# Optimization experiments

Measured on AMD Instinct MI355X. Metric: run time of the kernel, lower is better.

## Reference

```python
import jax, jax.numpy as jnp
import numpy as np

B, S, D, H = 2, 2048, 1024, 16
HD = D // H  # 64
LN_EPS = 1e-5


def setup_inputs() -> dict:
    key = jax.random.key(0)
    ks = jax.random.split(key, 10)
    s = 0.02
    return {
        "x": jax.random.normal(ks[0], (B, S, D), jnp.float32),
        "cdr_bias": jax.random.normal(ks[1], (B, S), jnp.float32),
        "Wq": jax.random.normal(ks[2], (D, D), jnp.float32) * s,
        "bq": jnp.zeros((D,), jnp.float32),
        "Wk": jax.random.normal(ks[3], (D, D), jnp.float32) * s,
        "bk": jnp.zeros((D,), jnp.float32),
        "Wv": jax.random.normal(ks[4], (D, D), jnp.float32) * s,
        "bv": jnp.zeros((D,), jnp.float32),
        "Wo": jax.random.normal(ks[5], (D, D), jnp.float32) * s,
        "bo": jnp.zeros((D,), jnp.float32),
        "gamma": jnp.ones((D,), jnp.float32),
        "beta": jnp.zeros((D,), jnp.float32),
        "cdr_weight": jnp.asarray(1.0, jnp.float32),
    }


def _rotate_half(t):
    # interleaved rotate: [-x2_0, x1_0, -x2_1, x1_1, ...] matching torch stack+reshape
    t1 = t[..., ::2]
    t2 = t[..., 1::2]
    return jnp.stack((-t2, t1), axis=-1).reshape(t.shape)


def reference(x, cdr_bias, Wq, bq, Wk, bk, Wv, bv, Wo, bo, gamma, beta, cdr_weight):
    b, s, d = x.shape

    # RoPE tables (faithful to original: sin/cos concatenated, rotate_half interleaved)
    pos = jnp.arange(s, dtype=x.dtype)
    inv_freq = 1.0 / (10000.0 ** (jnp.arange(0, HD, 2, dtype=x.dtype) / HD))
    sinusoid = pos[:, None] * inv_freq[None, :]              # [S, HD/2]
    sin_pos = jnp.concatenate([jnp.sin(sinusoid)] * 2, -1)   # [S, HD]
    cos_pos = jnp.concatenate([jnp.cos(sinusoid)] * 2, -1)
    sin_pos = sin_pos[None, None]                            # [1,1,S,HD]
    cos_pos = cos_pos[None, None]

    def heads(t):
        return t.reshape(b, s, H, HD).transpose(0, 2, 1, 3)  # [B,H,S,HD]

    Q = heads(x @ Wq + bq)
    K = heads(x @ Wk + bk)
    V = heads(x @ Wv + bv)

    Q = Q * cos_pos + _rotate_half(Q) * sin_pos
    K = K * cos_pos + _rotate_half(K) * sin_pos

    scores = jnp.einsum("bhqd,bhkd->bhqk", Q, K) / jnp.sqrt(jnp.asarray(HD, x.dtype))
    scores = scores + cdr_bias[:, None, None, :] * cdr_weight  # additive key-side bias
    probs = jax.nn.softmax(scores, axis=-1)                    # dropout = identity (eval)

    attn = jnp.einsum("bhqk,bhkd->bhqd", probs, V)
    attn = attn.transpose(0, 2, 1, 3).reshape(b, s, d)
    out = attn @ Wo + bo

    res = x + out
    mu = jnp.mean(res, axis=-1, keepdims=True)
    var = jnp.mean(jnp.square(res - mu), axis=-1, keepdims=True)
    return (res - mu) / jnp.sqrt(var + LN_EPS) * gamma + beta
```

## Files before the change

### kernel.cpp

```cpp
#include <hip/hip_runtime.h>
#include <hip/hip_bf16.h>
#include <math.h>

#define BB 2
#define SS 2048
#define DD 1024
#define HH 16
#define HD 64
#define MM (BB*SS)
#define LN_EPS 1e-5f
#define KVB 64
#define LOG2E 1.44269504088896340736f

typedef unsigned short u16;
typedef __attribute__((ext_vector_type(8))) short short8;
typedef __attribute__((ext_vector_type(4))) float f32x4;
typedef __attribute__((ext_vector_type(4))) unsigned short u16x4;

__device__ __forceinline__ u16 f2bf(float f) {
    union { __hip_bfloat16 h; u16 u; } cv;
    cv.h = __float2bfloat16(f);
    return cv.u;
}

__device__ __forceinline__ float exp2_(float x) {
    float r;
    asm("v_exp_f32 %0, %1" : "=v"(r) : "v"(x));
    return r;
}

__device__ __forceinline__ void gload16(const void* g, void* l) {
    __builtin_amdgcn_global_load_lds(
        (const __attribute__((address_space(1))) void*)g,
        (__attribute__((address_space(3))) void*)l, 16, 0, 0);
}

__global__ __launch_bounds__(256) void k_prep(
        const float* __restrict__ x,
        const float* __restrict__ Wq, const float* __restrict__ Wk,
        const float* __restrict__ Wv, const float* __restrict__ Wo,
        const float* __restrict__ cdr_bias, const float* __restrict__ cw,
        u16* __restrict__ xb, u16* __restrict__ wqkvt, u16* __restrict__ wot,
        float* __restrict__ cosb, float* __restrict__ sinb, float* __restrict__ biasf) {
    __shared__ float t[32][33];
    int bz = blockIdx.x, tid = threadIdx.x;
    if (bz < 4096) {
        int i = bz * 256 + tid;
        float4 v = ((const float4*)x)[i];
        u16x4 o;
        o[0] = f2bf(v.x); o[1] = f2bf(v.y); o[2] = f2bf(v.z); o[3] = f2bf(v.w);
        ((u16x4*)xb)[i] = o;
    } else if (bz < 8192) {
        int zb = bz - 4096;
        int z = zb >> 10, rem = zb & 1023;
        int k0 = (rem & 31) * 32, n0 = (rem >> 5) * 32;
        const float* W = (z == 0) ? Wq : (z == 1) ? Wk : (z == 2) ? Wv : Wo;
        u16* dst = (z < 3) ? (wqkvt + (size_t)z * DD * DD) : wot;
        int tx = tid & 31, ty = tid >> 5;
        #pragma unroll
        for (int r = 0; r < 32; r += 8)
            t[ty + r][tx] = W[(size_t)(k0 + ty + r) * DD + n0 + tx];
        __syncthreads();
        #pragma unroll
        for (int r = 0; r < 32; r += 8)
            dst[(size_t)(n0 + ty + r) * DD + k0 + tx] = f2bf(t[tx][ty + r]);
    } else {
        int idx = (bz - 8192) * 256 + tid;
        if (idx < BB * SS) biasf[idx] = cdr_bias[idx] * cw[0] * LOG2E;
        int s = idx >> 6, j = idx & 63;
        double invf = pow(10000.0, -((double)(2 * (j & 31))) / 64.0);
        double ang = (double)s * invf;
        cosb[idx] = (float)cos(ang);
        sinb[idx] = (float)sin(ang);
    }
}

#define STAGE_T(A_PTR, B_PTR, T)                                               \
    {                                                                          \
        u16* Ab = Alds + ((T) % 3) * 4096;                                     \
        u16* Bb = Blds + ((T) % 3) * 4096;                                     \
        _Pragma("unroll")                                                      \
        for (int i_ = 0; i_ < 2; i_++) {                                       \
            int p_ = i_ * 256 + tid;                                           \
            int row_ = p_ >> 2, c_ = p_ & 3;                                   \
            gload16(A_PTR + (size_t)(bm + row_) * DD + (T) * 32 + ((c_ ^ (row_ & 3)) << 3), Ab + p_ * 8); \
            gload16(B_PTR + (size_t)(bn + row_) * DD + (T) * 32 + ((c_ ^ (row_ & 3)) << 3), Bb + p_ * 8); \
        }                                                                      \
    }

#define GEMM_PIPE3(A_PTR, B_PTR)                                               \
    f32x4 acc[4][4] = {};                                                      \
    STAGE_T(A_PTR, B_PTR, 0)                                                   \
    STAGE_T(A_PTR, B_PTR, 1)                                                   \
    for (int kt = 0; kt < 32; kt++) {                                          \
        if (kt < 31) asm volatile("s_waitcnt vmcnt(4)" ::: "memory");          \
        else         asm volatile("s_waitcnt vmcnt(0)" ::: "memory");          \
        __builtin_amdgcn_s_barrier();                                          \
        const u16* Acur = Alds + (kt % 3) * 4096;                              \
        const u16* Bcur = Blds + (kt % 3) * 4096;                              \
        short8 a[4], b[4];                                                     \
        int rch = (lg ^ (lr & 3)) << 3;                                        \
        _Pragma("unroll")                                                      \
        for (int i = 0; i < 4; i++) {                                          \
            a[i] = *(const short8*)(Acur + (wm * 64 + i * 16 + lr) * 32 + rch); \
            b[i] = *(const short8*)(Bcur + (wn * 64 + i * 16 + lr) * 32 + rch); \
        }                                                                      \
        if (kt + 2 < 32) STAGE_T(A_PTR, B_PTR, kt + 2)                         \
        __builtin_amdgcn_s_setprio(1);                                         \
        _Pragma("unroll")                                                      \
        for (int i = 0; i < 4; i++)                                            \
            _Pragma("unroll")                                                  \
            for (int j = 0; j < 4; j++)                                        \
                acc[i][j] = __builtin_amdgcn_mfma_f32_16x16x32_bf16(a[i], b[j], acc[i][j], 0, 0, 0); \
        __builtin_amdgcn_s_setprio(0);                                         \
    }                                                                          \
    __syncthreads();

__global__ __launch_bounds__(256, 3) void k_gemm_qkv(
        const u16* __restrict__ xb, const u16* __restrict__ wqkvt,
        const float* __restrict__ bq, const float* __restrict__ bk, const float* __restrict__ bv,
        const float* __restrict__ cosb, const float* __restrict__ sinb,
        u16* __restrict__ q, u16* __restrict__ k, u16* __restrict__ vt) {
    __shared__ u16 SMEM[24576];
    u16* Alds = SMEM;
    u16* Blds = SMEM + 12288;
    int tid = threadIdx.x;
    int lane = tid & 63, wid = tid >> 6;
    int wm = wid >> 1, wn = wid & 1;
    int bm = blockIdx.x * 128, bn = blockIdx.y * 128;
    int lr = lane & 15, lg = lane >> 4;

    GEMM_PIPE3(xb, wqkvt)

    int w = bn >> 10;
    if (w == 2) {
        u16* Tr = SMEM;
        #pragma unroll
        for (int j = 0; j < 4; j++) {
            int n_l = wn * 64 + j * 16 + lr;
            float bias = bv[(bn - 2048) + n_l];
            #pragma unroll
            for (int i = 0; i < 4; i++) {
                ushort4 pk;
                pk.x = f2bf(acc[i][j][0] + bias);
                pk.y = f2bf(acc[i][j][1] + bias);
                pk.z = f2bf(acc[i][j][2] + bias);
                pk.w = f2bf(acc[i][j][3] + bias);
                *(ushort4*)&Tr[n_l * 136 + wm * 64 + i * 16 + lg * 4] = pk;
            }
        }
        __syncthreads();
        int n_r = tid >> 1, hf = tid & 1;
        int nglob = (bn - 2048) + n_r;
        int b_ = bm >> 11;
        size_t vbase = ((size_t)(b_ * HH + (nglob >> 6)) * HD + (nglob & 63)) * SS
                     + (bm & 2047) + hf * 64;
        #pragma unroll
        for (int ii = 0; ii < 8; ii++)
            *(short8*)(vt + vbase + ii * 8) = *(const short8*)&Tr[n_r * 136 + hf * 64 + ii * 8];
    } else {
        int m0 = bm + wm * 64, n0 = bn + wn * 64;
        #pragma unroll
        for (int j = 0; j < 4; j++) {
            int n = n0 + j * 16 + lr;
            int n1 = n & 1023;
            int h = n1 >> 6, d = n1 & 63;
            float bias = (w == 0) ? bq[n1] : bk[n1];
            #pragma unroll
            for (int i = 0; i < 4; i++) {
                #pragma unroll
                for (int r = 0; r < 4; r++) {
                    int m = m0 + i * 16 + lg * 4 + r;
                    int b_ = m >> 11, s = m & 2047;
                    float val = acc[i][j][r] + bias;
                    float part = __shfl_xor(val, 1);
                    float c = cosb[s * 64 + d], sn = sinb[s * 64 + d];
                    float rot = (d & 1) ? part : -part;
                    val = val * c + rot * sn;
                    size_t bh = (size_t)(b_ * HH + h);
                    if (w == 0)
                        q[(bh * SS + s) * HD + d] = f2bf(val * (0.125f * LOG2E));
                    else
                        k[(bh * SS + s) * HD + d] = f2bf(val);
                }
            }
        }
    }
}

__global__ __launch_bounds__(256, 3) void k_gemm_o(
        const u16* __restrict__ attnb, const u16* __restrict__ wot,
        const float* __restrict__ bo, const float* __restrict__ x,
        float* __restrict__ res) {
    __shared__ u16 SMEM[24576];
    u16* Alds = SMEM;
    u16* Blds = SMEM + 12288;
    int tid = threadIdx.x;
    int lane = tid & 63, wid = tid >> 6;
    int wm = wid >> 1, wn = wid & 1;
    int bm = blockIdx.x * 128, bn = blockIdx.y * 128;
    int lr = lane & 15, lg = lane >> 4;

    GEMM_PIPE3(attnb, wot)

    int m0 = bm + wm * 64, n0 = bn + wn * 64;
    #pragma unroll
    for (int i = 0; i < 4; i++) {
        #pragma unroll
        for (int j = 0; j < 4; j++) {
            int n = n0 + j * 16 + lr;
            #pragma unroll
            for (int r = 0; r < 4; r++) {
                int m = m0 + i * 16 + lg * 4 + r;
                res[(size_t)m * DD + n] = acc[i][j][r] + bo[n] + x[(size_t)m * DD + n];
            }
        }
    }
}

__device__ __forceinline__ void stage64x64(const u16* __restrict__ gbase, size_t rstride,
                                           u16* lds, int tid) {
    int row = tid >> 3, c = tid & 7;
    gload16(gbase + (size_t)row * rstride + (size_t)((c ^ (row & 7)) << 3), lds + tid * 8);
}

__global__ __launch_bounds__(512, 4) void k_attn(
        const u16* __restrict__ q, const u16* __restrict__ kkv, const u16* __restrict__ vt,
        const float* __restrict__ biasf, u16* __restrict__ attnb) {
    __shared__ u16 Klds[2][64 * 64];
    __shared__ u16 Vlds[2][64 * 64];
    __shared__ u16 plds[8][16][72];

    int tid = threadIdx.x;
    int lane = tid & 63, wid = tid >> 6;
    int flat = blockIdx.y * gridDim.x + blockIdx.x;
    int bh = (flat & 7) * 4 + (flat >> 7);
    int qb = (flat >> 3) & 15;
    int b_ = bh >> 4, h = bh & 15;
    int q0 = qb * 128 + wid * 16;
    int lr = lane & 15, lg = lane >> 4;

    short8 qa[2];
    #pragma unroll
    for (int ks = 0; ks < 2; ks++)
        qa[ks] = *(const short8*)(q + ((size_t)bh * SS + q0 + lr) * HD + ks * 32 + lg * 8);

    stage64x64(kkv + ((size_t)bh * SS) * HD, HD, Klds[0], tid);
    stage64x64(vt + ((size_t)bh * HD) * SS, SS, Vlds[0], tid);
    __syncthreads();

    f32x4 acco[4] = {};
    f32x4 acS = {};
    const float* bias_b = biasf + (size_t)b_ * SS;
    short8 vone;
    #pragma unroll
    for (int j = 0; j < 8; j++) vone[j] = (short)0x3F80;

    for (int t = 0; t < SS / KVB; t++) {
        int cur = t & 1;
        if (t + 1 < SS / KVB) {
            int kv1 = (t + 1) * KVB;
            stage64x64(kkv + ((size_t)bh * SS + kv1) * HD, HD, Klds[cur ^ 1], tid);
            stage64x64(vt + ((size_t)bh * HD) * SS + kv1, SS, Vlds[cur ^ 1], tid);
        }
        const u16* Kc = Klds[cur];
        const u16* Vc = Vlds[cur];

        f32x4 s_[4];
        #pragma unroll
        for (int n = 0; n < 4; n++) {
            float4 b4 = *(const float4*)(bias_b + t * KVB + n * 16 + lg * 4);
            s_[n][0] = b4.x; s_[n][1] = b4.y; s_[n][2] = b4.z; s_[n][3] = b4.w;
        }

        short8 kf[4][2], vf[4][2];
        #pragma unroll
        for (int n = 0; n < 4; n++) {
            int row = n * 16 + lr;
            #pragma unroll
            for (int ks = 0; ks < 2; ks++)
                kf[n][ks] = *(const short8*)(Kc + row * 64 + (((ks * 4 + lg) ^ (lr & 7)) << 3));
        }
        #pragma unroll
        for (int dt = 0; dt < 4; dt++) {
            int row = dt * 16 + lr;
            #pragma unroll
            for (int kt = 0; kt < 2; kt++)
                vf[dt][kt] = *(const short8*)(Vc + row * 64 + (((kt * 4 + lg) ^ (lr & 7)) << 3));
        }

        __builtin_amdgcn_s_setprio(1);
        #pragma unroll
        for (int n = 0; n < 4; n++) {
            s_[n] = __builtin_amdgcn_mfma_f32_16x16x32_bf16(kf[n][0], qa[0], s_[n], 0, 0, 0);
            s_[n] = __builtin_amdgcn_mfma_f32_16x16x32_bf16(kf[n][1], qa[1], s_[n], 0, 0, 0);
        }
        __builtin_amdgcn_s_setprio(0);

        #pragma unroll
        for (int n = 0; n < 4; n++) {
            ushort4 pk;
            pk.x = f2bf(exp2_(s_[n][0]));
            pk.y = f2bf(exp2_(s_[n][1]));
            pk.z = f2bf(exp2_(s_[n][2]));
            pk.w = f2bf(exp2_(s_[n][3]));
            *(ushort4*)&plds[wid][lr][n * 16 + lg * 4] = pk;
        }
        asm volatile("s_waitcnt lgkmcnt(0)" ::: "memory");
        __builtin_amdgcn_s_setprio(1);
        #pragma unroll
        for (int kt = 0; kt < 2; kt++) {
            short8 pa = *(const short8*)&plds[wid][lr][kt * 32 + lg * 8];
            #pragma unroll
            for (int dt = 0; dt < 4; dt++)
                acco[dt] = __builtin_amdgcn_mfma_f32_16x16x32_bf16(pa, vf[dt][kt], acco[dt], 0, 0, 0);
            acS = __builtin_amdgcn_mfma_f32_16x16x32_bf16(pa, vone, acS, 0, 0, 0);
        }
        __builtin_amdgcn_s_setprio(0);
        __syncthreads();
    }

    float linv[4];
    #pragma unroll
    for (int r = 0; r < 4; r++) linv[r] = 1.f / acS[r];
    #pragma unroll
    for (int dt = 0; dt < 4; dt++)
        #pragma unroll
        for (int r = 0; r < 4; r++)
            attnb[((size_t)b_ * SS + q0 + lg * 4 + r) * DD + h * HD + dt * 16 + lr] =
                f2bf(acco[dt][r] * linv[r]);
}

__global__ __launch_bounds__(256) void k_ln(const float* __restrict__ res,
        const float* __restrict__ gamma, const float* __restrict__ beta,
        float* __restrict__ out) {
    int row = blockIdx.x, tid = threadIdx.x;
    float4 v = ((const float4*)(res + (size_t)row * DD))[tid];
    float s = v.x + v.y + v.z + v.w;
    float ss = v.x * v.x + v.y * v.y + v.z * v.z + v.w * v.w;
    #pragma unroll
    for (int off = 32; off; off >>= 1) { s += __shfl_xor(s, off); ss += __shfl_xor(ss, off); }
    __shared__ float sbuf[8];
    int wid = tid >> 6, lane = tid & 63;
    if (lane == 0) { sbuf[wid] = s; sbuf[4 + wid] = ss; }
    __syncthreads();
    s = sbuf[0] + sbuf[1] + sbuf[2] + sbuf[3];
    ss = sbuf[4] + sbuf[5] + sbuf[6] + sbuf[7];
    float mu = s * (1.f / DD);
    float var = ss * (1.f / DD) - mu * mu;
    float rstd = rsqrtf(var + LN_EPS);
    float4 g = ((const float4*)gamma)[tid];
    float4 be = ((const float4*)beta)[tid];
    float4 o;
    o.x = (v.x - mu) * rstd * g.x + be.x;
    o.y = (v.y - mu) * rstd * g.y + be.y;
    o.z = (v.z - mu) * rstd * g.z + be.z;
    o.w = (v.w - mu) * rstd * g.w + be.w;
    ((float4*)(out + (size_t)row * DD))[tid] = o;
}

extern "C" void kernel_launch(void* const* d_in, const int* in_sizes, int n_in,
                              void* d_out, int out_size, void* d_ws, size_t ws_size,
                              hipStream_t stream) {
    const float* x        = (const float*)d_in[0];
    const float* cdr_bias = (const float*)d_in[1];
    const float* Wq       = (const float*)d_in[2];
    const float* bq       = (const float*)d_in[3];
    const float* Wk       = (const float*)d_in[4];
    const float* bk       = (const float*)d_in[5];
    const float* Wv       = (const float*)d_in[6];
    const float* bv       = (const float*)d_in[7];
    const float* Wo       = (const float*)d_in[8];
    const float* bo       = (const float*)d_in[9];
    const float* gamma    = (const float*)d_in[10];
    const float* beta     = (const float*)d_in[11];
    const float* cw       = (const float*)d_in[12];

    char* ws = (char*)d_ws;
    const size_t MB = 1048576;
    u16*   xb     = (u16*)(ws + 0);
    u16*   wqkvt  = (u16*)(ws + 8 * MB);
    u16*   wot    = (u16*)(ws + 14 * MB);
    u16*   qb     = (u16*)(ws + 16 * MB);
    u16*   kb     = (u16*)(ws + 24 * MB);
    u16*   vtb    = (u16*)(ws + 32 * MB);
    u16*   attnb  = (u16*)(ws + 40 * MB);
    float* res    = (float*)(ws + 48 * MB);
    float* biasf  = (float*)(ws + 48 * MB);
    float* cosb   = (float*)(ws + 64 * MB);
    float* sinb   = (float*)(ws + 64 * MB + 524288);

    k_prep     <<<8704, 256, 0, stream>>>(x, Wq, Wk, Wv, Wo, cdr_bias, cw,
                                          xb, wqkvt, wot, cosb, sinb, biasf);
    k_gemm_qkv <<<dim3(32, 24), 256, 0, stream>>>(xb, wqkvt, bq, bk, bv, cosb, sinb, qb, kb, vtb);
    k_attn     <<<dim3(16, 32), 512, 0, stream>>>(qb, kb, vtb, biasf, attnb);
    k_gemm_o   <<<dim3(32, 8), 256, 0, stream>>>(attnb, wot, bo, x, res);
    k_ln       <<<4096, 256, 0, stream>>>(res, gamma, beta, (float*)d_out);
}
```

Before: 123.7 us.

## Process two 16-row query fragments per wave in attention with 256-thread blocks

The attention kernel now runs 4 waves per block instead of 8, and each wave handles 32 query rows as two 16-row fragments. The K/V fragments read from LDS are reused across both fragments, which halves LDS fragment reads and the per-block staging thread count. The cost is more registers per wave (two sets of accumulators and Q fragments), a launch bound of 2 blocks per CU, and less wave-level parallelism for hiding latency.

```diff
diff --git a/kernel.cpp b/kernel.cpp
--- a/kernel.cpp
+++ b/kernel.cpp
@@ -218,18 +218,22 @@
     }
 }
 
-__device__ __forceinline__ void stage64x64(const u16* __restrict__ gbase, size_t rstride,
-                                           u16* lds, int tid) {
-    int row = tid >> 3, c = tid & 7;
-    gload16(gbase + (size_t)row * rstride + (size_t)((c ^ (row & 7)) << 3), lds + tid * 8);
-}
-
-__global__ __launch_bounds__(512, 4) void k_attn(
+__device__ __forceinline__ void stage64x64_256(const u16* __restrict__ gbase, size_t rstride,
+                                               u16* lds, int tid) {
+    #pragma unroll
+    for (int i = 0; i < 2; i++) {
+        int L = i * 256 + tid;
+        int row = L >> 3, c = L & 7;
+        gload16(gbase + (size_t)row * rstride + (size_t)((c ^ (row & 7)) << 3), lds + L * 8);
+    }
+}
+
+__global__ __launch_bounds__(256, 2) void k_attn(
         const u16* __restrict__ q, const u16* __restrict__ kkv, const u16* __restrict__ vt,
         const float* __restrict__ biasf, u16* __restrict__ attnb) {
     __shared__ u16 Klds[2][64 * 64];
     __shared__ u16 Vlds[2][64 * 64];
-    __shared__ u16 plds[8][16][72];
+    __shared__ u16 plds[4][32][72];
 
     int tid = threadIdx.x;
     int lane = tid & 63, wid = tid >> 6;
@@ -237,20 +241,22 @@
     int bh = (flat & 7) * 4 + (flat >> 7);
     int qb = (flat >> 3) & 15;
     int b_ = bh >> 4, h = bh & 15;
-    int q0 = qb * 128 + wid * 16;
+    int q0 = qb * 128 + wid * 32;
     int lr = lane & 15, lg = lane >> 4;
 
-    short8 qa[2];
-    #pragma unroll
-    for (int ks = 0; ks < 2; ks++)
-        qa[ks] = *(const short8*)(q + ((size_t)bh * SS + q0 + lr) * HD + ks * 32 + lg * 8);
-
-    stage64x64(kkv + ((size_t)bh * SS) * HD, HD, Klds[0], tid);
-    stage64x64(vt + ((size_t)bh * HD) * SS, SS, Vlds[0], tid);
+    short8 qa[2][2];
+    #pragma unroll
+    for (int qf = 0; qf < 2; qf++)
+        #pragma unroll
+        for (int ks = 0; ks < 2; ks++)
+            qa[qf][ks] = *(const short8*)(q + ((size_t)bh * SS + q0 + qf * 16 + lr) * HD + ks * 32 + lg * 8);
+
+    stage64x64_256(kkv + ((size_t)bh * SS) * HD, HD, Klds[0], tid);
+    stage64x64_256(vt + ((size_t)bh * HD) * SS, SS, Vlds[0], tid);
     __syncthreads();
 
-    f32x4 acco[4] = {};
-    f32x4 acS = {};
+    f32x4 acco[2][4] = {};
+    f32x4 acS[2] = {};
     const float* bias_b = biasf + (size_t)b_ * SS;
     short8 vone;
     #pragma unroll
@@ -260,18 +266,16 @@
         int cur = t & 1;
         if (t + 1 < SS / KVB) {
             int kv1 = (t + 1) * KVB;
-            stage64x64(kkv + ((size_t)bh * SS + kv1) * HD, HD, Klds[cur ^ 1], tid);
-            stage64x64(vt + ((size_t)bh * HD) * SS + kv1, SS, Vlds[cur ^ 1], tid);
+            stage64x64_256(kkv + ((size_t)bh * SS + kv1) * HD, HD, Klds[cur ^ 1], tid);
+            stage64x64_256(vt + ((size_t)bh * HD) * SS + kv1, SS, Vlds[cur ^ 1], tid);
         }
         const u16* Kc = Klds[cur];
         const u16* Vc = Vlds[cur];
 
-        f32x4 s_[4];
-        #pragma unroll
-        for (int n = 0; n < 4; n++) {
-            float4 b4 = *(const float4*)(bias_b + t * KVB + n * 16 + lg * 4);
-            s_[n][0] = b4.x; s_[n][1] = b4.y; s_[n][2] = b4.z; s_[n][3] = b4.w;
-        }
+        float4 bb[4];
+        #pragma unroll
+        for (int n = 0; n < 4; n++)
+            bb[n] = *(const float4*)(bias_b + t * KVB + n * 16 + lg * 4);
 
         short8 kf[4][2], vf[4][2];
         #pragma unroll
@@ -289,46 +293,57 @@
                 vf[dt][kt] = *(const short8*)(Vc + row * 64 + (((kt * 4 + lg) ^ (lr & 7)) << 3));
         }
 
-        __builtin_amdgcn_s_setprio(1);
-        #pragma unroll
-        for (int n = 0; n < 4; n++) {
-            s_[n] = __builtin_amdgcn_mfma_f32_16x16x32_bf16(kf[n][0], qa[0], s_[n], 0, 0, 0);
-            s_[n] = __builtin_amdgcn_mfma_f32_16x16x32_bf16(kf[n][1], qa[1], s_[n], 0, 0, 0);
-        }
-        __builtin_amdgcn_s_setprio(0);
-
-        #pragma unroll
-        for (int n = 0; n < 4; n++) {
-            ushort4 pk;
-            pk.x = f2bf(exp2_(s_[n][0]));
-            pk.y = f2bf(exp2_(s_[n][1]));
-            pk.z = f2bf(exp2_(s_[n][2]));
-            pk.w = f2bf(exp2_(s_[n][3]));
-            *(ushort4*)&plds[wid][lr][n * 16 + lg * 4] = pk;
-        }
-        asm volatile("s_waitcnt lgkmcnt(0)" ::: "memory");
-        __builtin_amdgcn_s_setprio(1);
-        #pragma unroll
-        for (int kt = 0; kt < 2; kt++) {
-            short8 pa = *(const short8*)&plds[wid][lr][kt * 32 + lg * 8];
-            #pragma unroll
-            for (int dt = 0; dt < 4; dt++)
-                acco[dt] = __builtin_amdgcn_mfma_f32_16x16x32_bf16(pa, vf[dt][kt], acco[dt], 0, 0, 0);
-            acS = __builtin_amdgcn_mfma_f32_16x16x32_bf16(pa, vone, acS, 0, 0, 0);
-        }
-        __builtin_amdgcn_s_setprio(0);
+        #pragma unroll
+        for (int qf = 0; qf < 2; qf++) {
+            f32x4 s_[4];
+            #pragma unroll
+            for (int n = 0; n < 4; n++) {
+                s_[n][0] = bb[n].x; s_[n][1] = bb[n].y; s_[n][2] = bb[n].z; s_[n][3] = bb[n].w;
+            }
+            __builtin_amdgcn_s_setprio(1);
+            #pragma unroll
+            for (int n = 0; n < 4; n++) {
+                s_[n] = __builtin_amdgcn_mfma_f32_16x16x32_bf16(kf[n][0], qa[qf][0], s_[n], 0, 0, 0);
+                s_[n] = __builtin_amdgcn_mfma_f32_16x16x32_bf16(kf[n][1], qa[qf][1], s_[n], 0, 0, 0);
+            }
+            __builtin_amdgcn_s_setprio(0);
+
+            #pragma unroll
+            for (int n = 0; n < 4; n++) {
+                ushort4 pk;
+                pk.x = f2bf(exp2_(s_[n][0]));
+                pk.y = f2bf(exp2_(s_[n][1]));
+                pk.z = f2bf(exp2_(s_[n][2]));
+                pk.w = f2bf(exp2_(s_[n][3]));
+                *(ushort4*)&plds[wid][qf * 16 + lr][n * 16 + lg * 4] = pk;
+            }
+            asm volatile("s_waitcnt lgkmcnt(0)" ::: "memory");
+            __builtin_amdgcn_s_setprio(1);
+            #pragma unroll
+            for (int kt = 0; kt < 2; kt++) {
+                short8 pa = *(const short8*)&plds[wid][qf * 16 + lr][kt * 32 + lg * 8];
+                #pragma unroll
+                for (int dt = 0; dt < 4; dt++)
+                    acco[qf][dt] = __builtin_amdgcn_mfma_f32_16x16x32_bf16(pa, vf[dt][kt], acco[qf][dt], 0, 0, 0);
+                acS[qf] = __builtin_amdgcn_mfma_f32_16x16x32_bf16(pa, vone, acS[qf], 0, 0, 0);
+            }
+            __builtin_amdgcn_s_setprio(0);
+        }
         __syncthreads();
     }
 
-    float linv[4];
-    #pragma unroll
-    for (int r = 0; r < 4; r++) linv[r] = 1.f / acS[r];
-    #pragma unroll
-    for (int dt = 0; dt < 4; dt++)
-        #pragma unroll
-        for (int r = 0; r < 4; r++)
-            attnb[((size_t)b_ * SS + q0 + lg * 4 + r) * DD + h * HD + dt * 16 + lr] =
-                f2bf(acco[dt][r] * linv[r]);
+    #pragma unroll
+    for (int qf = 0; qf < 2; qf++) {
+        float linv[4];
+        #pragma unroll
+        for (int r = 0; r < 4; r++) linv[r] = 1.f / acS[qf][r];
+        #pragma unroll
+        for (int dt = 0; dt < 4; dt++)
+            #pragma unroll
+            for (int r = 0; r < 4; r++)
+                attnb[((size_t)b_ * SS + q0 + qf * 16 + lg * 4 + r) * DD + h * HD + dt * 16 + lr] =
+                    f2bf(acco[qf][dt][r] * linv[r]);
+    }
 }
 
 __global__ __launch_bounds__(256) void k_ln(const float* __restrict__ res,
@@ -393,7 +408,7 @@
     k_prep     <<<8704, 256, 0, stream>>>(x, Wq, Wk, Wv, Wo, cdr_bias, cw,
                                           xb, wqkvt, wot, cosb, sinb, biasf);
     k_gemm_qkv <<<dim3(32, 24), 256, 0, stream>>>(xb, wqkvt, bq, bk, bv, cosb, sinb, qb, kb, vtb);
-    k_attn     <<<dim3(16, 32), 512, 0, stream>>>(qb, kb, vtb, biasf, attnb);
+    k_attn     <<<dim3(16, 32), 256, 0, stream>>>(qb, kb, vtb, biasf, attnb);
     k_gemm_o   <<<dim3(32, 8), 256, 0, stream>>>(attnb, wot, bo, x, res);
     k_ln       <<<4096, 256, 0, stream>>>(res, gamma, beta, (float*)d_out);
 }
```

Result: no change. 125.4 us (+1.4%).

## Load K/V fragments directly from global memory in attention, drop LDS staging

Applied to the files above, without the earlier changes.

The attention kernel no longer stages K and V tiles through double-buffered shared memory. Each wave now loads its MFMA fragments straight from global memory, relying on L1/L2 to serve the reuse across the block's waves. Blocks shrink to 256 threads covering 64 query rows, the grid doubles, and the per-tile __syncthreads is removed. This cuts LDS traffic and barrier stalls, but each wave now issues more global loads with no explicit prefetch, so latency hiding depends on occupancy.

```diff
diff --git a/kernel.cpp b/kernel.cpp
--- a/kernel.cpp
+++ b/kernel.cpp
@@ -218,75 +218,57 @@
     }
 }
 
-__device__ __forceinline__ void stage64x64(const u16* __restrict__ gbase, size_t rstride,
-                                           u16* lds, int tid) {
-    int row = tid >> 3, c = tid & 7;
-    gload16(gbase + (size_t)row * rstride + (size_t)((c ^ (row & 7)) << 3), lds + tid * 8);
-}
-
-__global__ __launch_bounds__(512, 4) void k_attn(
+__global__ __launch_bounds__(256, 4) void k_attn(
         const u16* __restrict__ q, const u16* __restrict__ kkv, const u16* __restrict__ vt,
         const float* __restrict__ biasf, u16* __restrict__ attnb) {
-    __shared__ u16 Klds[2][64 * 64];
-    __shared__ u16 Vlds[2][64 * 64];
-    __shared__ u16 plds[8][16][72];
+    __shared__ u16 plds[4][16][72];
 
     int tid = threadIdx.x;
     int lane = tid & 63, wid = tid >> 6;
     int flat = blockIdx.y * gridDim.x + blockIdx.x;
-    int bh = (flat & 7) * 4 + (flat >> 7);
-    int qb = (flat >> 3) & 15;
+    int w_ = flat >> 3;
+    int bh = (flat & 7) * 4 + (w_ >> 5);
+    int qb = w_ & 31;
     int b_ = bh >> 4, h = bh & 15;
-    int q0 = qb * 128 + wid * 16;
+    int q0 = qb * 64 + wid * 16;
     int lr = lane & 15, lg = lane >> 4;
 
     short8 qa[2];
     #pragma unroll
     for (int ks = 0; ks < 2; ks++)
         qa[ks] = *(const short8*)(q + ((size_t)bh * SS + q0 + lr) * HD + ks * 32 + lg * 8);
-
-    stage64x64(kkv + ((size_t)bh * SS) * HD, HD, Klds[0], tid);
-    stage64x64(vt + ((size_t)bh * HD) * SS, SS, Vlds[0], tid);
-    __syncthreads();
 
     f32x4 acco[4] = {};
     f32x4 acS = {};
     const float* bias_b = biasf + (size_t)b_ * SS;
+    const u16* kbase = kkv + (size_t)bh * SS * HD;
+    const u16* vbase = vt + (size_t)bh * HD * SS;
     short8 vone;
     #pragma unroll
     for (int j = 0; j < 8; j++) vone[j] = (short)0x3F80;
 
     for (int t = 0; t < SS / KVB; t++) {
-        int cur = t & 1;
-        if (t + 1 < SS / KVB) {
-            int kv1 = (t + 1) * KVB;
-            stage64x64(kkv + ((size_t)bh * SS + kv1) * HD, HD, Klds[cur ^ 1], tid);
-            stage64x64(vt + ((size_t)bh * HD) * SS + kv1, SS, Vlds[cur ^ 1], tid);
-        }
-        const u16* Kc = Klds[cur];
-        const u16* Vc = Vlds[cur];
+        short8 kf[4][2], vf[4][2];
+        #pragma unroll
+        for (int n = 0; n < 4; n++) {
+            const u16* kr = kbase + (size_t)(t * KVB + n * 16 + lr) * HD;
+            #pragma unroll
+            for (int ks = 0; ks < 2; ks++)
+                kf[n][ks] = *(const short8*)(kr + ks * 32 + lg * 8);
+        }
+        #pragma unroll
+        for (int dt = 0; dt < 4; dt++) {
+            const u16* vr = vbase + (size_t)(dt * 16 + lr) * SS + t * KVB;
+            #pragma unroll
+            for (int kt = 0; kt < 2; kt++)
+                vf[dt][kt] = *(const short8*)(vr + kt * 32 + lg * 8);
+        }
 
         f32x4 s_[4];
         #pragma unroll
         for (int n = 0; n < 4; n++) {
             float4 b4 = *(const float4*)(bias_b + t * KVB + n * 16 + lg * 4);
             s_[n][0] = b4.x; s_[n][1] = b4.y; s_[n][2] = b4.z; s_[n][3] = b4.w;
-        }
-
-        short8 kf[4][2], vf[4][2];
-        #pragma unroll
-        for (int n = 0; n < 4; n++) {
-            int row = n * 16 + lr;
-            #pragma unroll
-            for (int ks = 0; ks < 2; ks++)
-                kf[n][ks] = *(const short8*)(Kc + row * 64 + (((ks * 4 + lg) ^ (lr & 7)) << 3));
-        }
-        #pragma unroll
-        for (int dt = 0; dt < 4; dt++) {
-            int row = dt * 16 + lr;
-            #pragma unroll
-            for (int kt = 0; kt < 2; kt++)
-                vf[dt][kt] = *(const short8*)(Vc + row * 64 + (((kt * 4 + lg) ^ (lr & 7)) << 3));
         }
 
         __builtin_amdgcn_s_setprio(1);
@@ -317,7 +299,6 @@
             acS = __builtin_amdgcn_mfma_f32_16x16x32_bf16(pa, vone, acS, 0, 0, 0);
         }
         __builtin_amdgcn_s_setprio(0);
-        __syncthreads();
     }
 
     float linv[4];
@@ -393,7 +374,7 @@
     k_prep     <<<8704, 256, 0, stream>>>(x, Wq, Wk, Wv, Wo, cdr_bias, cw,
                                           xb, wqkvt, wot, cosb, sinb, biasf);
     k_gemm_qkv <<<dim3(32, 24), 256, 0, stream>>>(xb, wqkvt, bq, bk, bv, cosb, sinb, qb, kb, vtb);
-    k_attn     <<<dim3(16, 32), 512, 0, stream>>>(qb, kb, vtb, biasf, attnb);
+    k_attn     <<<dim3(32, 32), 256, 0, stream>>>(qb, kb, vtb, biasf, attnb);
     k_gemm_o   <<<dim3(32, 8), 256, 0, stream>>>(attnb, wot, bo, x, res);
     k_ln       <<<4096, 256, 0, stream>>>(res, gamma, beta, (float*)d_out);
 }
```

Measured after the change: 314.8 us. +154.4%, slower.
